# Performance work log

Measured on AMD Instinct MI355X. Metric: run time of the kernel, lower is better.

The kernel has to match this reference:

```python
import jax, jax.numpy as jnp
import numpy as np

SCALE = 4          # sigma // 2 with sigma = 8
EP = 1e-20         # epsilon used by xcorr_torch


def _pad(x, w):
    # zero-pad last two (spatial) dims by w on each side
    cfg = [(0, 0)] * (x.ndim - 2) + [(w, w), (w, w)]
    return jnp.pad(x, cfg)


def _box(x, w):
    # sliding 2w x 2w box sum via 2D integral image (cumsum trick),
    # matching xcorr_torch's cumsum/difference formulation.
    c = jnp.cumsum(jnp.cumsum(x, axis=-1), axis=-2)
    return (c[..., 2 * w:, 2 * w:] - c[..., :-2 * w, 2 * w:]
            - c[..., 2 * w:, :-2 * w] + c[..., :-2 * w, :-2 * w])


def _xcorr(a, b, w):
    # local (windowed) normalized cross-correlation field.
    # a: [B,C,1,H,W], b: [B,1,L,H,W]; broadcasting gives [B,C,L,H,W]
    a_mu = _box(_pad(a, w), w) / (4.0 * w * w)
    b_mu = _box(_pad(b, w), w) / (4.0 * w * w)
    ac = _pad(a - a_mu, w)
    bc = _pad(b - b_mu, w)
    sii = jnp.maximum(_box(ac * ac, w), EP)   # clip lower bound; upper clip at
    sjj = jnp.maximum(_box(bc * bc, w), EP)   # tensor max in torch is a no-op
    sij = _box(ac * bc, w)                    # [B,C,L,H,W]
    return sij / (jnp.sqrt(sii * sjj) + EP)


def setup_inputs() -> dict:
    key = jax.random.key(0)
    k1, k2 = jax.random.split(key)
    outputs = jax.random.uniform(k1, (4, 6, 512, 512), dtype=jnp.float32)
    labels = jax.random.uniform(k2, (4, 4, 512, 512), dtype=jnp.float32)
    return {"outputs": outputs, "labels": labels}


def reference(outputs, labels):
    w = SCALE
    a = outputs[:, :, None]            # [B,C,1,H,W]
    b = labels[:, None, :]             # [B,1,L,H,W]
    cc = _xcorr(a, b, w)               # [B,C,L,H,W] (torch loop over L, vectorized)
    Y = jnp.maximum(cc, -1.0)          # torch.clamp(min=-1)
    Y = jnp.max(Y, axis=2)             # amax over label channels -> [B,C,H,W]
    Y = jnp.clip(Y, -1.0, 1.0)
    X = 1.0 - Y
    return (jnp.mean(X), jnp.mean(X, axis=(2, 3)))
```

## Files before the change

### kernel.cpp

```cpp
#include <hip/hip_runtime.h>
#include <hip/hip_fp16.h>

#define HH 512
#define WW 512
#define HW (HH*WW)
#define EPV 1e-20f


__device__ __forceinline__ float bpl(int addr, float v) {
    return __int_as_float(__builtin_amdgcn_ds_bpermute(addr, __float_as_int(v)));
}
__device__ __forceinline__ int rcl(int r) { return min(max(r, 0), HH - 1); }

__device__ __forceinline__ float4 h2f4(uint2 r) {
    __half2 lo = *(__half2*)&r.x, hi = *(__half2*)&r.y;
    float2 a = __half22float2(lo), b = __half22float2(hi);
    return make_float4(a.x, a.y, b.x, b.y);
}
__device__ __forceinline__ uint2 f2h4(float4 v) {
    __half2 lo = __floats2half2_rn(v.x, v.y);
    __half2 hi = __floats2half2_rn(v.z, v.w);
    uint2 r;
    r.x = *(unsigned int*)&lo;
    r.y = *(unsigned int*)&hi;
    return r;
}

__device__ __forceinline__ float4 winC(float4 v, int aL1, int aR1) {
    float pre2 = v.x + v.y, pre3 = pre2 + v.z, g = pre3 + v.w;
    float suf2 = v.z + v.w, suf3 = v.y + suf2;
    float Ls1 = bpl(aL1, v.w), Ls2 = bpl(aL1, suf2), Ls3 = bpl(aL1, suf3);
    float Rp1 = bpl(aR1, v.x), Rp2 = bpl(aR1, pre2), Rp3 = bpl(aR1, pre3);
    float Rg  = bpl(aR1, g);
    return make_float4(Ls3 + g + Rp1, Ls2 + g + Rp2, Ls1 + g + Rp3, g + Rg);
}
__device__ __forceinline__ float4 winR(float4 v, int aR1, int aR2) {
    float pre2 = v.x + v.y, pre3 = pre2 + v.z, g = pre3 + v.w;
    float suf2 = v.z + v.w, suf3 = v.y + suf2;
    float G1 = bpl(aR1, g);
    float P1 = bpl(aR2, v.x), P2 = bpl(aR2, pre2), P3 = bpl(aR2, pre3);
    float G2 = bpl(aR2, g);
    return make_float4(suf3 + G1 + P1, suf2 + G1 + P2, v.w + G1 + P3, G1 + G2);
}

__global__ __launch_bounds__(64, 2) void prep_f4(
    const float* __restrict__ outs, const float* __restrict__ labs,
    __half* __restrict__ ac, __half* __restrict__ rs, float* __restrict__ wsum)
{
    const int l  = threadIdx.x;
    if (blockIdx.x == 0 && blockIdx.y == 0 && blockIdx.z == 0 && l < 24)
        wsum[l * 64] = 0.f;
    const int s  = blockIdx.x;
    const int x0 = (s == 0) ? 0 : (s == 1 ? 232 : 468);
    const int y0 = 16 * blockIdx.y;
    const int z  = blockIdx.z;

    const float* src = (z < 24) ? outs + z * HW : labs + (z - 24) * HW;
    __half* acd = ac + z * HW;
    __half* rsd = rs + z * HW;

    const int   bcol0 = x0 - 4 + 4 * l;
    const int   bcol  = min(max(bcol0, 0), WW - 4);
    const float cmask = (bcol0 >= 0 && bcol0 <= WW - 4) ? 1.f : 0.f;
    const int   ocol0 = x0 + 4 * l;
    const int   aL1 = ((l - 1) & 63) << 2;
    const int   aR1 = ((l + 1) & 63) << 2;
    const int   aR2 = ((l + 2) & 63) << 2;
    const bool stA = (l >= 1 && l <= 60 && bcol0 >= 0 && bcol0 <= WW - 4);
    const bool stS = (l >= ((x0 == 0) ? 0 : 1) && l <= 59 && ocol0 <= WW - 4);

    float4 fifo[4];
    fifo[0] = *(const float4*)&src[rcl(y0 - 7) * WW + bcol];
    fifo[1] = *(const float4*)&src[rcl(y0 - 6) * WW + bcol];
    fifo[2] = *(const float4*)&src[rcl(y0 - 5) * WW + bcol];
    fifo[3] = *(const float4*)&src[rcl(y0 - 4) * WW + bcol];

    float4 araw[4], haR[8], rgS[8];
    float4 VA = make_float4(0,0,0,0), Vq = make_float4(0,0,0,0);
    #pragma unroll
    for (int k = 0; k < 4; ++k) araw[k] = make_float4(0,0,0,0);
    #pragma unroll
    for (int k = 0; k < 8; ++k) { haR[k] = make_float4(0,0,0,0); rgS[k] = make_float4(0,0,0,0); }

    auto step = [&](const int t, const int kk) {
        const int   r  = y0 - 7 + t;
        const float rm = (r >= 0 && r < HH) ? cmask : 0.f;
        float4 raw = fifo[kk & 3];
        float4 av  = make_float4(raw.x*rm, raw.y*rm, raw.z*rm, raw.w*rm);
        if (t <= 26) fifo[kk & 3] = *(const float4*)&src[rcl(r + 4) * WW + bcol];

        float4 h = winC(av, aL1, aR1);
        VA.x += h.x - haR[kk].x; VA.y += h.y - haR[kk].y;
        VA.z += h.z - haR[kk].z; VA.w += h.w - haR[kk].w;
        haR[kk] = h;

        float4 aold = araw[kk & 3]; araw[kk & 3] = av;
        const int   c  = r - 4;
        const float cm = (c >= 0 && c < HH) ? cmask : 0.f;
        float4 acv = make_float4((aold.x - VA.x*(1.f/64.f))*cm,
                                 (aold.y - VA.y*(1.f/64.f))*cm,
                                 (aold.z - VA.z*(1.f/64.f))*cm,
                                 (aold.w - VA.w*(1.f/64.f))*cm);
        if (t >= 11 && t <= 26) {
            if (stA) *(uint2*)&acd[c * WW + bcol0] = f2h4(acv);
        }
        float4 sq = make_float4(acv.x*acv.x, acv.y*acv.y, acv.z*acv.z, acv.w*acv.w);
        Vq.x += sq.x - rgS[kk].x; Vq.y += sq.y - rgS[kk].y;
        Vq.z += sq.z - rgS[kk].z; Vq.w += sq.w - rgS[kk].w;
        rgS[kk] = sq;
        if (t >= 15 && t <= 30) {
            const int y = c - 4;
            float4 h2 = winR(Vq, aR1, aR2);
            float4 rv = make_float4(
                fminf(__frsqrt_rn(fmaxf(h2.x, EPV)), 60000.f),
                fminf(__frsqrt_rn(fmaxf(h2.y, EPV)), 60000.f),
                fminf(__frsqrt_rn(fmaxf(h2.z, EPV)), 60000.f),
                fminf(__frsqrt_rn(fmaxf(h2.w, EPV)), 60000.f));
            if (stS) *(uint2*)&rsd[y * WW + ocol0] = f2h4(rv);
        }
    };
    for (int it = 0; it < 4; ++it) {
        const int t0 = it * 8;
        #pragma unroll
        for (int kk = 0; kk < 8; ++kk) step(t0 + kk, kk);
    }
}

__global__ __launch_bounds__(64, 2) void ncc_f4(
    const __half* __restrict__ ac, const __half* __restrict__ rs,
    float* __restrict__ wsum)
{
    const int l   = threadIdx.x;
    const int n   = blockIdx.x;
    const int xcd = n & 7;
    const int p   = n >> 3;
    const int zq  = p / 192;
    const int rem = p - 192 * zq;
    const int seg = rem / 3;
    const int stp = rem - 3 * seg;
    const int x0  = 240 * stp;
    const int y0  = 8 * seg;
    const int z   = 3 * xcd + zq;
    const int b   = z / 6;

    const __half* acp = ac + z * HW;
    const __half* sip = rs + z * HW;
    const __half* bcp[4]; const __half* sjp[4];
    #pragma unroll
    for (int j = 0; j < 4; ++j) {
        bcp[j] = ac + (24 + b * 4 + j) * HW;
        sjp[j] = rs + (24 + b * 4 + j) * HW;
    }

    const int   bcol0 = x0 - 4 + 4 * l;
    const int   bcol  = min(max(bcol0, 0), WW - 4);
    const float cmask = (bcol0 >= 0 && bcol0 <= WW - 4) ? 1.f : 0.f;
    const int   ocol0 = x0 + 4 * l;
    const int   ocol  = min(ocol0, WW - 4);
    const float om    = (l <= 59 && ocol0 <= WW - 4) ? 1.f : 0.f;
    const int   aR1 = ((l + 1) & 63) << 2;
    const int   aR2 = ((l + 2) & 63) << 2;

    uint2 fa[2], fb[4][2];
    uint2 faO[2], fbO[4][2];
    {
        const int r0 = rcl(y0 - 3), r1 = rcl(y0 - 2);
        fa[0]  = *(const uint2*)&acp[r0 * WW + bcol];
        fa[1]  = *(const uint2*)&acp[r1 * WW + bcol];
        faO[0] = fa[0];
        faO[1] = fa[1];
        #pragma unroll
        for (int j = 0; j < 4; ++j) {
            fb[j][0]  = *(const uint2*)&bcp[j][r0 * WW + bcol];
            fb[j][1]  = *(const uint2*)&bcp[j][r1 * WW + bcol];
            fbO[j][0] = fb[j][0];
            fbO[j][1] = fb[j][1];
        }
    }

    float4 Vp[4];
    uint2 psiB[2], psjB[2][4];
    float4 xs = make_float4(0,0,0,0);
    #pragma unroll
    for (int j = 0; j < 4; ++j) Vp[j] = make_float4(0,0,0,0);
    #pragma unroll
    for (int q = 0; q < 2; ++q) {
        psiB[q] = make_uint2(0, 0);
        #pragma unroll
        for (int j = 0; j < 4; ++j) psjB[q][j] = make_uint2(0, 0);
    }

    auto step = [&](const int t, const int kk) {
        const int   c  = y0 - 3 + t;
        const float rm = (c >= 0 && c < HH) ? cmask : 0.f;
        float4 av = h2f4(fa[kk & 1]);
        av = make_float4(av.x*rm, av.y*rm, av.z*rm, av.w*rm);
        float4 bv0 = h2f4(fb[0][kk & 1]), bv1 = h2f4(fb[1][kk & 1]);
        float4 bv2 = h2f4(fb[2][kk & 1]), bv3 = h2f4(fb[3][kk & 1]);
        if (t <= 12) {
            const int rn = rcl(c + 2);
            fa[kk & 1] = *(const uint2*)&acp[rn * WW + bcol];
            #pragma unroll
            for (int j = 0; j < 4; ++j)
                fb[j][kk & 1] = *(const uint2*)&bcp[j][rn * WW + bcol];
        }
        Vp[0].x += av.x*bv0.x; Vp[0].y += av.y*bv0.y; Vp[0].z += av.z*bv0.z; Vp[0].w += av.w*bv0.w;
        Vp[1].x += av.x*bv1.x; Vp[1].y += av.y*bv1.y; Vp[1].z += av.z*bv1.z; Vp[1].w += av.w*bv1.w;
        Vp[2].x += av.x*bv2.x; Vp[2].y += av.y*bv2.y; Vp[2].z += av.z*bv2.z; Vp[2].w += av.w*bv2.w;
        Vp[3].x += av.x*bv3.x; Vp[3].y += av.y*bv3.y; Vp[3].z += av.z*bv3.z; Vp[3].w += av.w*bv3.w;
        if (t >= 8) {
            const int   co  = c - 8;
            const float rmO = (co >= 0) ? cmask : 0.f;
            float4 avO = h2f4(faO[kk & 1]);
            avO = make_float4(avO.x*rmO, avO.y*rmO, avO.z*rmO, avO.w*rmO);
            float4 bo0 = h2f4(fbO[0][kk & 1]), bo1 = h2f4(fbO[1][kk & 1]);
            float4 bo2 = h2f4(fbO[2][kk & 1]), bo3 = h2f4(fbO[3][kk & 1]);
            Vp[0].x -= avO.x*bo0.x; Vp[0].y -= avO.y*bo0.y; Vp[0].z -= avO.z*bo0.z; Vp[0].w -= avO.w*bo0.w;
            Vp[1].x -= avO.x*bo1.x; Vp[1].y -= avO.y*bo1.y; Vp[1].z -= avO.z*bo1.z; Vp[1].w -= avO.w*bo1.w;
            Vp[2].x -= avO.x*bo2.x; Vp[2].y -= avO.y*bo2.y; Vp[2].z -= avO.z*bo2.z; Vp[2].w -= avO.w*bo2.w;
            Vp[3].x -= avO.x*bo3.x; Vp[3].y -= avO.y*bo3.y; Vp[3].z -= avO.z*bo3.z; Vp[3].w -= avO.w*bo3.w;
        }
        if (t >= 6 && t <= 12) {
            const int ro = rcl(c - 6);
            faO[kk & 1] = *(const uint2*)&acp[ro * WW + bcol];
            #pragma unroll
            for (int j = 0; j < 4; ++j)
                fbO[j][kk & 1] = *(const uint2*)&bcp[j][ro * WW + bcol];
        }

        if (t >= 7) {
            const int   y  = y0 + t - 7;
            const float em = (y < HH) ? om : 0.f;
            const float4 psi = h2f4(psiB[t & 1]);
            float mmx = -1.f, mmy = -1.f, mmz = -1.f, mmw = -1.f;
            #pragma unroll
            for (int j = 0; j < 4; ++j) {
                float4 hj = winR(Vp[j], aR1, aR2);
                float4 sj = h2f4(psjB[t & 1][j]);
                mmx = fmaxf(mmx, hj.x * (psi.x * sj.x));
                mmy = fmaxf(mmy, hj.y * (psi.y * sj.y));
                mmz = fmaxf(mmz, hj.z * (psi.z * sj.z));
                mmw = fmaxf(mmw, hj.w * (psi.w * sj.w));
            }
            xs.x += em * (1.f - fminf(mmx, 1.f));
            xs.y += em * (1.f - fminf(mmy, 1.f));
            xs.z += em * (1.f - fminf(mmz, 1.f));
            xs.w += em * (1.f - fminf(mmw, 1.f));
        }
        if (t >= 5 && t <= 12) {
            const int yn = min(y0 + t - 5, HH - 1);
            psiB[t & 1] = *(const uint2*)&sip[yn * WW + ocol];
            #pragma unroll
            for (int j = 0; j < 4; ++j)
                psjB[t & 1][j] = *(const uint2*)&sjp[j][yn * WW + ocol];
        }
    };
    #pragma unroll
    for (int t = 0; t < 15; ++t) step(t, t & 7);

    float xt = xs.x + xs.y + xs.z + xs.w;
    #pragma unroll
    for (int off = 32; off > 0; off >>= 1) xt += __shfl_down(xt, off);
    if (l == 0) atomicAdd(&wsum[z * 64], xt);
}

__global__ void fin_f4(const float* __restrict__ wsum, float* __restrict__ out)
{
    const int l = threadIdx.x;
    float v = (l < 24) ? wsum[l * 64] : 0.f;
    if (l < 24) out[1 + l] = v * (1.f / (float)HW);
    #pragma unroll
    for (int off = 32; off > 0; off >>= 1) v += __shfl_down(v, off);
    if (l == 0) out[0] = v * (1.f / (24.f * (float)HW));
}

extern "C" void kernel_launch(void* const* d_in, const int* in_sizes, int n_in,
                              void* d_out, int out_size, void* d_ws, size_t ws_size,
                              hipStream_t stream) {
    const float* outs = (const float*)d_in[0];
    const float* labs = (const float*)d_in[1];
    float* out = (float*)d_out;
    float* ws  = (float*)d_ws;

    __half* acw  = (__half*)ws;
    __half* rsw  = (__half*)ws + 40 * HW;
    float*  wsum = ws + 40 * HW;

    prep_f4<<<dim3(3, 32, 40), 64, 0, stream>>>(outs, labs, acw, rsw, wsum);
    ncc_f4<<<dim3(4608, 1, 1), 64, 0, stream>>>(acw, rsw, wsum);
    fin_f4<<<dim3(1, 1, 1), 64, 0, stream>>>(wsum, out);
}
```

Measured before the change: 123.9 us.

## Process 8 columns per lane so one wave covers a full 512-wide row

```diff
diff --git a/kernel.cpp b/kernel.cpp
--- a/kernel.cpp
+++ b/kernel.cpp
@@ -25,98 +25,129 @@
     r.y = *(unsigned int*)&hi;
     return r;
 }
-
-__device__ __forceinline__ float4 winC(float4 v, int aL1, int aR1) {
-    float pre2 = v.x + v.y, pre3 = pre2 + v.z, g = pre3 + v.w;
-    float suf2 = v.z + v.w, suf3 = v.y + suf2;
-    float Ls1 = bpl(aL1, v.w), Ls2 = bpl(aL1, suf2), Ls3 = bpl(aL1, suf3);
-    float Rp1 = bpl(aR1, v.x), Rp2 = bpl(aR1, pre2), Rp3 = bpl(aR1, pre3);
-    float Rg  = bpl(aR1, g);
-    return make_float4(Ls3 + g + Rp1, Ls2 + g + Rp2, Ls1 + g + Rp3, g + Rg);
-}
-__device__ __forceinline__ float4 winR(float4 v, int aR1, int aR2) {
-    float pre2 = v.x + v.y, pre3 = pre2 + v.z, g = pre3 + v.w;
-    float suf2 = v.z + v.w, suf3 = v.y + suf2;
-    float G1 = bpl(aR1, g);
-    float P1 = bpl(aR2, v.x), P2 = bpl(aR2, pre2), P3 = bpl(aR2, pre3);
-    float G2 = bpl(aR2, g);
-    return make_float4(suf3 + G1 + P1, suf2 + G1 + P2, v.w + G1 + P3, G1 + G2);
-}
-
-__global__ __launch_bounds__(64, 2) void prep_f4(
+__device__ __forceinline__ uint4 pack8(float4 a, float4 b) {
+    uint2 lo = f2h4(a), hi = f2h4(b);
+    return make_uint4(lo.x, lo.y, hi.x, hi.y);
+}
+__device__ __forceinline__ void unpack8(uint4 r, float4& a, float4& b) {
+    a = h2f4(make_uint2(r.x, r.y));
+    b = h2f4(make_uint2(r.z, r.w));
+}
+
+__global__ __launch_bounds__(64, 2) void prep_f8(
     const float* __restrict__ outs, const float* __restrict__ labs,
     __half* __restrict__ ac, __half* __restrict__ rs, float* __restrict__ wsum)
 {
-    const int l  = threadIdx.x;
-    if (blockIdx.x == 0 && blockIdx.y == 0 && blockIdx.z == 0 && l < 24)
+    const int l = threadIdx.x;
+    if (blockIdx.x == 0 && blockIdx.y == 0 && l < 24)
         wsum[l * 64] = 0.f;
-    const int s  = blockIdx.x;
-    const int x0 = (s == 0) ? 0 : (s == 1 ? 232 : 468);
-    const int y0 = 16 * blockIdx.y;
-    const int z  = blockIdx.z;
+    const int y0 = 16 * blockIdx.x;
+    const int z  = blockIdx.y;
 
     const float* src = (z < 24) ? outs + z * HW : labs + (z - 24) * HW;
     __half* acd = ac + z * HW;
     __half* rsd = rs + z * HW;
 
-    const int   bcol0 = x0 - 4 + 4 * l;
-    const int   bcol  = min(max(bcol0, 0), WW - 4);
-    const float cmask = (bcol0 >= 0 && bcol0 <= WW - 4) ? 1.f : 0.f;
-    const int   ocol0 = x0 + 4 * l;
+    const int   col = 8 * l;
     const int   aL1 = ((l - 1) & 63) << 2;
     const int   aR1 = ((l + 1) & 63) << 2;
-    const int   aR2 = ((l + 2) & 63) << 2;
-    const bool stA = (l >= 1 && l <= 60 && bcol0 >= 0 && bcol0 <= WW - 4);
-    const bool stS = (l >= ((x0 == 0) ? 0 : 1) && l <= 59 && ocol0 <= WW - 4);
-
-    float4 fifo[4];
-    fifo[0] = *(const float4*)&src[rcl(y0 - 7) * WW + bcol];
-    fifo[1] = *(const float4*)&src[rcl(y0 - 6) * WW + bcol];
-    fifo[2] = *(const float4*)&src[rcl(y0 - 5) * WW + bcol];
-    fifo[3] = *(const float4*)&src[rcl(y0 - 4) * WW + bcol];
-
-    float4 araw[4], haR[8], rgS[8];
-    float4 VA = make_float4(0,0,0,0), Vq = make_float4(0,0,0,0);
-    #pragma unroll
-    for (int k = 0; k < 4; ++k) araw[k] = make_float4(0,0,0,0);
-    #pragma unroll
-    for (int k = 0; k < 8; ++k) { haR[k] = make_float4(0,0,0,0); rgS[k] = make_float4(0,0,0,0); }
+    const float lmE = (l > 0)  ? 1.f : 0.f;
+    const float rmE = (l < 63) ? 1.f : 0.f;
+
+    float4 fA[8], fB[8];
+    float4 foA[2], foB[2];
+    float4 gA[8], gB[8];
+    float4 VAa = {0,0,0,0}, VAb = {0,0,0,0};
+    float4 Vqa = {0,0,0,0}, Vqb = {0,0,0,0};
+    #pragma unroll
+    for (int k = 0; k < 8; ++k) {
+        gA[k] = make_float4(0,0,0,0); gB[k] = make_float4(0,0,0,0);
+        fA[k] = make_float4(0,0,0,0); fB[k] = make_float4(0,0,0,0);
+    }
+    foA[0] = foA[1] = foB[0] = foB[1] = make_float4(0,0,0,0);
+    {
+        const int pr[6] = { rcl(y0-7), rcl(y0-6), rcl(y0-11), rcl(y0-10),
+                            rcl(y0-9), rcl(y0-8) };
+        const int sl[6] = { 0, 1, 4, 5, 6, 7 };
+        #pragma unroll
+        for (int q = 0; q < 6; ++q) {
+            fA[sl[q]] = *(const float4*)&src[pr[q] * WW + col];
+            fB[sl[q]] = *(const float4*)&src[pr[q] * WW + col + 4];
+        }
+    }
 
     auto step = [&](const int t, const int kk) {
         const int   r  = y0 - 7 + t;
-        const float rm = (r >= 0 && r < HH) ? cmask : 0.f;
-        float4 raw = fifo[kk & 3];
-        float4 av  = make_float4(raw.x*rm, raw.y*rm, raw.z*rm, raw.w*rm);
-        if (t <= 26) fifo[kk & 3] = *(const float4*)&src[rcl(r + 4) * WW + bcol];
-
-        float4 h = winC(av, aL1, aR1);
-        VA.x += h.x - haR[kk].x; VA.y += h.y - haR[kk].y;
-        VA.z += h.z - haR[kk].z; VA.w += h.w - haR[kk].w;
-        haR[kk] = h;
-
-        float4 aold = araw[kk & 3]; araw[kk & 3] = av;
-        const int   c  = r - 4;
-        const float cm = (c >= 0 && c < HH) ? cmask : 0.f;
-        float4 acv = make_float4((aold.x - VA.x*(1.f/64.f))*cm,
-                                 (aold.y - VA.y*(1.f/64.f))*cm,
-                                 (aold.z - VA.z*(1.f/64.f))*cm,
-                                 (aold.w - VA.w*(1.f/64.f))*cm);
-        if (t >= 11 && t <= 26) {
-            if (stA) *(uint2*)&acd[c * WW + bcol0] = f2h4(acv);
-        }
-        float4 sq = make_float4(acv.x*acv.x, acv.y*acv.y, acv.z*acv.z, acv.w*acv.w);
-        Vq.x += sq.x - rgS[kk].x; Vq.y += sq.y - rgS[kk].y;
-        Vq.z += sq.z - rgS[kk].z; Vq.w += sq.w - rgS[kk].w;
-        rgS[kk] = sq;
-        if (t >= 15 && t <= 30) {
-            const int y = c - 4;
-            float4 h2 = winR(Vq, aR1, aR2);
-            float4 rv = make_float4(
-                fminf(__frsqrt_rn(fmaxf(h2.x, EPV)), 60000.f),
-                fminf(__frsqrt_rn(fmaxf(h2.y, EPV)), 60000.f),
-                fminf(__frsqrt_rn(fmaxf(h2.z, EPV)), 60000.f),
-                fminf(__frsqrt_rn(fmaxf(h2.w, EPV)), 60000.f));
-            if (stS) *(uint2*)&rsd[y * WW + ocol0] = f2h4(rv);
+        const float rm = (r >= 0 && r < HH) ? 1.f : 0.f;
+        {
+            float4 ra = fA[kk], rb = fB[kk];
+            VAa.x += ra.x*rm; VAa.y += ra.y*rm; VAa.z += ra.z*rm; VAa.w += ra.w*rm;
+            VAb.x += rb.x*rm; VAb.y += rb.y*rm; VAb.z += rb.z*rm; VAb.w += rb.w*rm;
+        }
+        if (t >= 8) {
+            const int   r8  = r - 8;
+            const float rm8 = (r8 >= 0 && r8 < HH) ? 1.f : 0.f;
+            float4 oa = foA[kk & 1], ob = foB[kk & 1];
+            VAa.x -= oa.x*rm8; VAa.y -= oa.y*rm8; VAa.z -= oa.z*rm8; VAa.w -= oa.w*rm8;
+            VAb.x -= ob.x*rm8; VAb.y -= ob.y*rm8; VAb.z -= ob.z*rm8; VAb.w -= ob.w*rm8;
+        }
+        if (t <= 28) {
+            const int rn = rcl(r + 2);
+            fA[(kk + 2) & 7] = *(const float4*)&src[rn * WW + col];
+            fB[(kk + 2) & 7] = *(const float4*)&src[rn * WW + col + 4];
+        }
+        if (t >= 6 && t <= 28) {
+            const int ro = rcl(r - 6);
+            foA[kk & 1] = *(const float4*)&src[ro * WW + col];
+            foB[kk & 1] = *(const float4*)&src[ro * WW + col + 4];
+        }
+        if (t >= 8) {
+            const int   c  = r - 4;
+            const float cm = (c >= 0 && c < HH) ? 1.f : 0.f;
+            float p1 = VAa.x, p2 = p1+VAa.y, p3 = p2+VAa.z, p4 = p3+VAa.w;
+            float p5 = p4+VAb.x, p6 = p5+VAb.y, p7 = p6+VAb.z, tt = p7+VAb.w;
+            float s1 = VAb.w, s2 = VAb.z+s1, s3 = VAb.y+s2;
+            float L1 = bpl(aL1, s1)*lmE, L2 = bpl(aL1, s2)*lmE, L3 = bpl(aL1, s3)*lmE;
+            float R1 = bpl(aR1, p1)*rmE, R2 = bpl(aR1, p2)*rmE;
+            float R3 = bpl(aR1, p3)*rmE, R4 = bpl(aR1, p4)*rmE;
+            float4 rc0 = fA[(kk + 4) & 7], rc1 = fB[(kk + 4) & 7];
+            float4 aL4, aH4;
+            aL4.x = (rc0.x - (L3+p5)     * (1.f/64.f)) * cm;
+            aL4.y = (rc0.y - (L2+p6)     * (1.f/64.f)) * cm;
+            aL4.z = (rc0.z - (L1+p7)     * (1.f/64.f)) * cm;
+            aL4.w = (rc0.w - tt          * (1.f/64.f)) * cm;
+            aH4.x = (rc1.x - (tt-p1+R1)  * (1.f/64.f)) * cm;
+            aH4.y = (rc1.y - (tt-p2+R2)  * (1.f/64.f)) * cm;
+            aH4.z = (rc1.z - (tt-p3+R3)  * (1.f/64.f)) * cm;
+            aH4.w = (rc1.w - (tt-p4+R4)  * (1.f/64.f)) * cm;
+            if (t >= 11 && t <= 26)
+                *(uint4*)&acd[c * WW + col] = pack8(aL4, aH4);
+            float4 qa = make_float4(aL4.x*aL4.x, aL4.y*aL4.y, aL4.z*aL4.z, aL4.w*aL4.w);
+            float4 qb = make_float4(aH4.x*aH4.x, aH4.y*aH4.y, aH4.z*aH4.z, aH4.w*aH4.w);
+            Vqa.x += qa.x - gA[kk].x; Vqa.y += qa.y - gA[kk].y;
+            Vqa.z += qa.z - gA[kk].z; Vqa.w += qa.w - gA[kk].w;
+            Vqb.x += qb.x - gB[kk].x; Vqb.y += qb.y - gB[kk].y;
+            Vqb.z += qb.z - gB[kk].z; Vqb.w += qb.w - gB[kk].w;
+            gA[kk] = qa; gB[kk] = qb;
+            if (t >= 15 && t <= 30) {
+                const int y = c - 4;
+                float q1 = Vqa.x, q2 = q1+Vqa.y, q3 = q2+Vqa.z, q4 = q3+Vqa.w;
+                float q5 = q4+Vqb.x, q6 = q5+Vqb.y, q7 = q6+Vqb.z, qt = q7+Vqb.w;
+                float T1 = bpl(aR1, q1)*rmE, T2 = bpl(aR1, q2)*rmE;
+                float T3 = bpl(aR1, q3)*rmE, T4 = bpl(aR1, q4)*rmE;
+                float T5 = bpl(aR1, q5)*rmE, T6 = bpl(aR1, q6)*rmE;
+                float T7 = bpl(aR1, q7)*rmE, Tg = bpl(aR1, qt)*rmE;
+                float4 rL, rH;
+                rL.x = fminf(__frsqrt_rn(fmaxf(qt-q1+T1, EPV)), 60000.f);
+                rL.y = fminf(__frsqrt_rn(fmaxf(qt-q2+T2, EPV)), 60000.f);
+                rL.z = fminf(__frsqrt_rn(fmaxf(qt-q3+T3, EPV)), 60000.f);
+                rL.w = fminf(__frsqrt_rn(fmaxf(qt-q4+T4, EPV)), 60000.f);
+                rH.x = fminf(__frsqrt_rn(fmaxf(qt-q5+T5, EPV)), 60000.f);
+                rH.y = fminf(__frsqrt_rn(fmaxf(qt-q6+T6, EPV)), 60000.f);
+                rH.z = fminf(__frsqrt_rn(fmaxf(qt-q7+T7, EPV)), 60000.f);
+                rH.w = fminf(__frsqrt_rn(fmaxf(Tg,       EPV)), 60000.f);
+                *(uint4*)&rsd[y * WW + col] = pack8(rL, rH);
+            }
         }
     };
     for (int it = 0; it < 4; ++it) {
@@ -126,7 +157,7 @@
     }
 }
 
-__global__ __launch_bounds__(64, 2) void ncc_f4(
+__global__ __launch_bounds__(64, 2) void ncc_f8(
     const __half* __restrict__ ac, const __half* __restrict__ rs,
     float* __restrict__ wsum)
 {
@@ -134,14 +165,11 @@
     const int n   = blockIdx.x;
     const int xcd = n & 7;
     const int p   = n >> 3;
-    const int zq  = p / 192;
-    const int rem = p - 192 * zq;
-    const int seg = rem / 3;
-    const int stp = rem - 3 * seg;
-    const int x0  = 240 * stp;
-    const int y0  = 8 * seg;
+    const int zq  = p >> 6;
+    const int seg = p & 63;
     const int z   = 3 * xcd + zq;
     const int b   = z / 6;
+    const int y0  = 8 * seg;
 
     const __half* acp = ac + z * HW;
     const __half* sip = rs + z * HW;
@@ -152,113 +180,140 @@
         sjp[j] = rs + (24 + b * 4 + j) * HW;
     }
 
-    const int   bcol0 = x0 - 4 + 4 * l;
-    const int   bcol  = min(max(bcol0, 0), WW - 4);
-    const float cmask = (bcol0 >= 0 && bcol0 <= WW - 4) ? 1.f : 0.f;
-    const int   ocol0 = x0 + 4 * l;
-    const int   ocol  = min(ocol0, WW - 4);
-    const float om    = (l <= 59 && ocol0 <= WW - 4) ? 1.f : 0.f;
+    const int   col = 8 * l;
     const int   aR1 = ((l + 1) & 63) << 2;
-    const int   aR2 = ((l + 2) & 63) << 2;
-
-    uint2 fa[2], fb[4][2];
-    uint2 faO[2], fbO[4][2];
+    const float rmE = (l < 63) ? 1.f : 0.f;
+
+    uint4 fa[2], fb[4][2];
+    uint4 faO[2], fbO[4][2];
     {
         const int r0 = rcl(y0 - 3), r1 = rcl(y0 - 2);
-        fa[0]  = *(const uint2*)&acp[r0 * WW + bcol];
-        fa[1]  = *(const uint2*)&acp[r1 * WW + bcol];
-        faO[0] = fa[0];
-        faO[1] = fa[1];
+        fa[0] = *(const uint4*)&acp[r0 * WW + col];
+        fa[1] = *(const uint4*)&acp[r1 * WW + col];
+        faO[0] = fa[0]; faO[1] = fa[1];
         #pragma unroll
         for (int j = 0; j < 4; ++j) {
-            fb[j][0]  = *(const uint2*)&bcp[j][r0 * WW + bcol];
-            fb[j][1]  = *(const uint2*)&bcp[j][r1 * WW + bcol];
-            fbO[j][0] = fb[j][0];
-            fbO[j][1] = fb[j][1];
-        }
-    }
-
-    float4 Vp[4];
-    uint2 psiB[2], psjB[2][4];
-    float4 xs = make_float4(0,0,0,0);
-    #pragma unroll
-    for (int j = 0; j < 4; ++j) Vp[j] = make_float4(0,0,0,0);
-    #pragma unroll
-    for (int q = 0; q < 2; ++q) {
-        psiB[q] = make_uint2(0, 0);
-        #pragma unroll
-        for (int j = 0; j < 4; ++j) psjB[q][j] = make_uint2(0, 0);
-    }
+            fb[j][0] = *(const uint4*)&bcp[j][r0 * WW + col];
+            fb[j][1] = *(const uint4*)&bcp[j][r1 * WW + col];
+            fbO[j][0] = fb[j][0]; fbO[j][1] = fb[j][1];
+        }
+    }
+
+    float4 VpL[4], VpH[4];
+    uint4 psiB[2], psjB[2][4];
+    float4 xsL = make_float4(0,0,0,0), xsH = make_float4(0,0,0,0);
+    #pragma unroll
+    for (int j = 0; j < 4; ++j) {
+        VpL[j] = make_float4(0,0,0,0); VpH[j] = make_float4(0,0,0,0);
+        psjB[0][j] = make_uint4(0,0,0,0); psjB[1][j] = make_uint4(0,0,0,0);
+    }
+    psiB[0] = make_uint4(0,0,0,0); psiB[1] = make_uint4(0,0,0,0);
 
     auto step = [&](const int t, const int kk) {
         const int   c  = y0 - 3 + t;
-        const float rm = (c >= 0 && c < HH) ? cmask : 0.f;
-        float4 av = h2f4(fa[kk & 1]);
-        av = make_float4(av.x*rm, av.y*rm, av.z*rm, av.w*rm);
-        float4 bv0 = h2f4(fb[0][kk & 1]), bv1 = h2f4(fb[1][kk & 1]);
-        float4 bv2 = h2f4(fb[2][kk & 1]), bv3 = h2f4(fb[3][kk & 1]);
+        const float rm = (c >= 0 && c < HH) ? 1.f : 0.f;
+        uint4 ar = fa[kk & 1];
+        uint4 br0 = fb[0][kk & 1], br1 = fb[1][kk & 1];
+        uint4 br2 = fb[2][kk & 1], br3 = fb[3][kk & 1];
+        uint4 arO = faO[kk & 1];
+        uint4 bo0 = fbO[0][kk & 1], bo1 = fbO[1][kk & 1];
+        uint4 bo2 = fbO[2][kk & 1], bo3 = fbO[3][kk & 1];
         if (t <= 12) {
             const int rn = rcl(c + 2);
-            fa[kk & 1] = *(const uint2*)&acp[rn * WW + bcol];
+            fa[kk & 1] = *(const uint4*)&acp[rn * WW + col];
             #pragma unroll
             for (int j = 0; j < 4; ++j)
-                fb[j][kk & 1] = *(const uint2*)&bcp[j][rn * WW + bcol];
-        }
-        Vp[0].x += av.x*bv0.x; Vp[0].y += av.y*bv0.y; Vp[0].z += av.z*bv0.z; Vp[0].w += av.w*bv0.w;
-        Vp[1].x += av.x*bv1.x; Vp[1].y += av.y*bv1.y; Vp[1].z += av.z*bv1.z; Vp[1].w += av.w*bv1.w;
-        Vp[2].x += av.x*bv2.x; Vp[2].y += av.y*bv2.y; Vp[2].z += av.z*bv2.z; Vp[2].w += av.w*bv2.w;
-        Vp[3].x += av.x*bv3.x; Vp[3].y += av.y*bv3.y; Vp[3].z += av.z*bv3.z; Vp[3].w += av.w*bv3.w;
-        if (t >= 8) {
-            const int   co  = c - 8;
-            const float rmO = (co >= 0) ? cmask : 0.f;
-            float4 avO = h2f4(faO[kk & 1]);
-            avO = make_float4(avO.x*rmO, avO.y*rmO, avO.z*rmO, avO.w*rmO);
-            float4 bo0 = h2f4(fbO[0][kk & 1]), bo1 = h2f4(fbO[1][kk & 1]);
-            float4 bo2 = h2f4(fbO[2][kk & 1]), bo3 = h2f4(fbO[3][kk & 1]);
-            Vp[0].x -= avO.x*bo0.x; Vp[0].y -= avO.y*bo0.y; Vp[0].z -= avO.z*bo0.z; Vp[0].w -= avO.w*bo0.w;
-            Vp[1].x -= avO.x*bo1.x; Vp[1].y -= avO.y*bo1.y; Vp[1].z -= avO.z*bo1.z; Vp[1].w -= avO.w*bo1.w;
-            Vp[2].x -= avO.x*bo2.x; Vp[2].y -= avO.y*bo2.y; Vp[2].z -= avO.z*bo2.z; Vp[2].w -= avO.w*bo2.w;
-            Vp[3].x -= avO.x*bo3.x; Vp[3].y -= avO.y*bo3.y; Vp[3].z -= avO.z*bo3.z; Vp[3].w -= avO.w*bo3.w;
+                fb[j][kk & 1] = *(const uint4*)&bcp[j][rn * WW + col];
         }
         if (t >= 6 && t <= 12) {
             const int ro = rcl(c - 6);
-            faO[kk & 1] = *(const uint2*)&acp[ro * WW + bcol];
+            faO[kk & 1] = *(const uint4*)&acp[ro * WW + col];
             #pragma unroll
             for (int j = 0; j < 4; ++j)
-                fbO[j][kk & 1] = *(const uint2*)&bcp[j][ro * WW + bcol];
-        }
-
-        if (t >= 7) {
-            const int   y  = y0 + t - 7;
-            const float em = (y < HH) ? om : 0.f;
-            const float4 psi = h2f4(psiB[t & 1]);
-            float mmx = -1.f, mmy = -1.f, mmz = -1.f, mmw = -1.f;
+                fbO[j][kk & 1] = *(const uint4*)&bcp[j][ro * WW + col];
+        }
+        {
+            float4 avL, avH; unpack8(ar, avL, avH);
+            avL.x *= rm; avL.y *= rm; avL.z *= rm; avL.w *= rm;
+            avH.x *= rm; avH.y *= rm; avH.z *= rm; avH.w *= rm;
+            float4 bL, bH;
+            unpack8(br0, bL, bH);
+            VpL[0].x += avL.x*bL.x; VpL[0].y += avL.y*bL.y; VpL[0].z += avL.z*bL.z; VpL[0].w += avL.w*bL.w;
+            VpH[0].x += avH.x*bH.x; VpH[0].y += avH.y*bH.y; VpH[0].z += avH.z*bH.z; VpH[0].w += avH.w*bH.w;
+            unpack8(br1, bL, bH);
+            VpL[1].x += avL.x*bL.x; VpL[1].y += avL.y*bL.y; VpL[1].z += avL.z*bL.z; VpL[1].w += avL.w*bL.w;
+            VpH[1].x += avH.x*bH.x; VpH[1].y += avH.y*bH.y; VpH[1].z += avH.z*bH.z; VpH[1].w += avH.w*bH.w;
+            unpack8(br2, bL, bH);
+            VpL[2].x += avL.x*bL.x; VpL[2].y += avL.y*bL.y; VpL[2].z += avL.z*bL.z; VpL[2].w += avL.w*bL.w;
+            VpH[2].x += avH.x*bH.x; VpH[2].y += avH.y*bH.y; VpH[2].z += avH.z*bH.z; VpH[2].w += avH.w*bH.w;
+            unpack8(br3, bL, bH);
+            VpL[3].x += avL.x*bL.x; VpL[3].y += avL.y*bL.y; VpL[3].z += avL.z*bL.z; VpL[3].w += avL.w*bL.w;
+            VpH[3].x += avH.x*bH.x; VpH[3].y += avH.y*bH.y; VpH[3].z += avH.z*bH.z; VpH[3].w += avH.w*bH.w;
+        }
+        if (t >= 8) {
+            const float rmO = ((c - 8) >= 0) ? 1.f : 0.f;
+            float4 avL, avH; unpack8(arO, avL, avH);
+            avL.x *= rmO; avL.y *= rmO; avL.z *= rmO; avL.w *= rmO;
+            avH.x *= rmO; avH.y *= rmO; avH.z *= rmO; avH.w *= rmO;
+            float4 bL, bH;
+            unpack8(bo0, bL, bH);
+            VpL[0].x -= avL.x*bL.x; VpL[0].y -= avL.y*bL.y; VpL[0].z -= avL.z*bL.z; VpL[0].w -= avL.w*bL.w;
+            VpH[0].x -= avH.x*bH.x; VpH[0].y -= avH.y*bH.y; VpH[0].z -= avH.z*bH.z; VpH[0].w -= avH.w*bH.w;
+            unpack8(bo1, bL, bH);
+            VpL[1].x -= avL.x*bL.x; VpL[1].y -= avL.y*bL.y; VpL[1].z -= avL.z*bL.z; VpL[1].w -= avL.w*bL.w;
+            VpH[1].x -= avH.x*bH.x; VpH[1].y -= avH.y*bH.y; VpH[1].z -= avH.z*bH.z; VpH[1].w -= avH.w*bH.w;
+            unpack8(bo2, bL, bH);
+            VpL[2].x -= avL.x*bL.x; VpL[2].y -= avL.y*bL.y; VpL[2].z -= avL.z*bL.z; VpL[2].w -= avL.w*bL.w;
+            VpH[2].x -= avH.x*bH.x; VpH[2].y -= avH.y*bH.y; VpH[2].z -= avH.z*bH.z; VpH[2].w -= avH.w*bH.w;
+            unpack8(bo3, bL, bH);
+            VpL[3].x -= avL.x*bL.x; VpL[3].y -= avL.y*bL.y; VpL[3].z -= avL.z*bL.z; VpL[3].w -= avL.w*bL.w;
+            VpH[3].x -= avH.x*bH.x; VpH[3].y -= avH.y*bH.y; VpH[3].z -= avH.z*bH.z; VpH[3].w -= avH.w*bH.w;
+        }
+        if (t >= 7 && t <= 14) {
+            float4 pL, pH; unpack8(psiB[t & 1], pL, pH);
+            float4 mmL = make_float4(-1,-1,-1,-1), mmH = make_float4(-1,-1,-1,-1);
             #pragma unroll
             for (int j = 0; j < 4; ++j) {
-                float4 hj = winR(Vp[j], aR1, aR2);
-                float4 sj = h2f4(psjB[t & 1][j]);
-                mmx = fmaxf(mmx, hj.x * (psi.x * sj.x));
-                mmy = fmaxf(mmy, hj.y * (psi.y * sj.y));
-                mmz = fmaxf(mmz, hj.z * (psi.z * sj.z));
-                mmw = fmaxf(mmw, hj.w * (psi.w * sj.w));
+                float p1 = VpL[j].x, p2 = p1+VpL[j].y, p3 = p2+VpL[j].z, p4 = p3+VpL[j].w;
+                float p5 = p4+VpH[j].x, p6 = p5+VpH[j].y, p7 = p6+VpH[j].z, tt = p7+VpH[j].w;
+                float R1 = bpl(aR1, p1)*rmE, R2 = bpl(aR1, p2)*rmE;
+                float R3 = bpl(aR1, p3)*rmE, R4 = bpl(aR1, p4)*rmE;
+                float R5 = bpl(aR1, p5)*rmE, R6 = bpl(aR1, p6)*rmE;
+                float R7 = bpl(aR1, p7)*rmE, Rg = bpl(aR1, tt)*rmE;
+                float4 sL, sH; unpack8(psjB[t & 1][j], sL, sH);
+                mmL.x = fmaxf(mmL.x, (tt-p1+R1) * (pL.x*sL.x));
+                mmL.y = fmaxf(mmL.y, (tt-p2+R2) * (pL.y*sL.y));
+                mmL.z = fmaxf(mmL.z, (tt-p3+R3) * (pL.z*sL.z));
+                mmL.w = fmaxf(mmL.w, (tt-p4+R4) * (pL.w*sL.w));
+                mmH.x = fmaxf(mmH.x, (tt-p5+R5) * (pH.x*sH.x));
+                mmH.y = fmaxf(mmH.y, (tt-p6+R6) * (pH.y*sH.y));
+                mmH.z = fmaxf(mmH.z, (tt-p7+R7) * (pH.z*sH.z));
+                mmH.w = fmaxf(mmH.w, Rg         * (pH.w*sH.w));
             }
-            xs.x += em * (1.f - fminf(mmx, 1.f));
-            xs.y += em * (1.f - fminf(mmy, 1.f));
-            xs.z += em * (1.f - fminf(mmz, 1.f));
-            xs.w += em * (1.f - fminf(mmw, 1.f));
+            xsL.x += 1.f - fminf(mmL.x, 1.f);
+            xsL.y += 1.f - fminf(mmL.y, 1.f);
+            xsL.z += 1.f - fminf(mmL.z, 1.f);
+            xsL.w += 1.f - fminf(mmL.w, 1.f);
+            xsH.x += 1.f - fminf(mmH.x, 1.f);
+            xsH.y += 1.f - fminf(mmH.y, 1.f);
+            xsH.z += 1.f - fminf(mmH.z, 1.f);
+            xsH.w += 1.f - fminf(mmH.w, 1.f);
         }
         if (t >= 5 && t <= 12) {
             const int yn = min(y0 + t - 5, HH - 1);
-            psiB[t & 1] = *(const uint2*)&sip[yn * WW + ocol];
+            psiB[t & 1] = *(const uint4*)&sip[yn * WW + col];
             #pragma unroll
             for (int j = 0; j < 4; ++j)
-                psjB[t & 1][j] = *(const uint2*)&sjp[j][yn * WW + ocol];
+                psjB[t & 1][j] = *(const uint4*)&sjp[j][yn * WW + col];
         }
     };
-    #pragma unroll
-    for (int t = 0; t < 15; ++t) step(t, t & 7);
-
-    float xt = xs.x + xs.y + xs.z + xs.w;
+    for (int it = 0; it < 2; ++it) {
+        const int t0 = it * 8;
+        #pragma unroll
+        for (int kk = 0; kk < 8; ++kk) step(t0 + kk, kk);
+    }
+
+    float xt = xsL.x + xsL.y + xsL.z + xsL.w + xsH.x + xsH.y + xsH.z + xsH.w;
     #pragma unroll
     for (int off = 32; off > 0; off >>= 1) xt += __shfl_down(xt, off);
     if (l == 0) atomicAdd(&wsum[z * 64], xt);
@@ -286,7 +341,7 @@
     __half* rsw  = (__half*)ws + 40 * HW;
     float*  wsum = ws + 40 * HW;
 
-    prep_f4<<<dim3(3, 32, 40), 64, 0, stream>>>(outs, labs, acw, rsw, wsum);
-    ncc_f4<<<dim3(4608, 1, 1), 64, 0, stream>>>(acw, rsw, wsum);
+    prep_f8<<<dim3(32, 40), 64, 0, stream>>>(outs, labs, acw, rsw, wsum);
+    ncc_f8<<<dim3(1536, 1, 1), 64, 0, stream>>>(acw, rsw, wsum);
     fin_f4<<<dim3(1, 1, 1), 64, 0, stream>>>(wsum, out);
 }
```

Result: slower. 153.8 us (+24.2%).
